# Performance work log

Hardware: AMD Instinct MI355X
Metric: run time of the kernel (lower is better)

## Reference

```python
import jax, jax.numpy as jnp
import numpy as np
from jax import lax

L = 3  # num_layers
H = 256  # hidden_size == embedding_size
V = 32000  # vocab (input_size / output_size)


def _lstm_layer(x, h0, c0, Wih, Whh, bih, bhh):
    # x: [T, B, H_in]; PyTorch gate order: i, f, g, o
    b = bih + bhh
    def step(carry, xt):
        h, c = carry
        gates = xt @ Wih.T + h @ Whh.T + b  # [B, 4H]
        i, f, g, o = jnp.split(gates, 4, axis=-1)
        c = jax.nn.sigmoid(f) * c + jax.nn.sigmoid(i) * jnp.tanh(g)
        h = jax.nn.sigmoid(o) * jnp.tanh(c)
        return (h, c), h
    (h, c), ys = lax.scan(step, (h0, c0), x)
    return ys, h, c


def _run_lstm(x, h0, c0, Wih, Whh, bih, bhh):
    hs, cs = [], []
    for l in range(L):
        x, h, c = _lstm_layer(x, h0[l], c0[l], Wih[l], Whh[l], bih[l], bhh[l])
        hs.append(h)
        cs.append(c)
    return x, jnp.stack(hs), jnp.stack(cs)


def setup_inputs() -> dict:
    key = jax.random.key(0)
    ks = jax.random.split(key, 16)
    s = 0.06  # ~ 1/sqrt(H) uniform scale of PyTorch LSTM init
    T_in, T_out, B = 64, 64, 64
    return {
        "inputs": jax.random.randint(ks[0], (T_in, B), 0, V, dtype=jnp.int64),
        "targets": jax.random.randint(ks[1], (T_out, B), 0, V, dtype=jnp.int64),
        "enc_emb": jax.random.normal(ks[2], (V, H), jnp.float32),
        "enc_Wih": jax.random.normal(ks[3], (L, 4 * H, H), jnp.float32) * s,
        "enc_Whh": jax.random.normal(ks[4], (L, 4 * H, H), jnp.float32) * s,
        "enc_bih": jax.random.normal(ks[5], (L, 4 * H), jnp.float32) * s,
        "enc_bhh": jax.random.normal(ks[6], (L, 4 * H), jnp.float32) * s,
        "hidden0": jax.random.normal(ks[7], (L, 1, H), jnp.float32) * s,
        "cell0": jax.random.normal(ks[8], (L, 1, H), jnp.float32) * s,
        "dec_emb": jax.random.normal(ks[9], (V, H), jnp.float32),
        "dec_Wih": jax.random.normal(ks[10], (L, 4 * H, H), jnp.float32) * s,
        "dec_Whh": jax.random.normal(ks[11], (L, 4 * H, H), jnp.float32) * s,
        "dec_bih": jax.random.normal(ks[12], (L, 4 * H), jnp.float32) * s,
        "dec_bhh": jax.random.normal(ks[13], (L, 4 * H), jnp.float32) * s,
        "fc_W": jax.random.normal(ks[14], (V, H), jnp.float32) * s,
        "fc_b": jax.random.normal(ks[15], (V,), jnp.float32) * s,
    }


def reference(inputs, targets, enc_emb, enc_Wih, enc_Whh, enc_bih, enc_bhh,
              hidden0, cell0, dec_emb, dec_Wih, dec_Whh, dec_bih, dec_bhh,
              fc_W, fc_b):
    B = inputs.shape[-1]
    # Encoder: learned init state broadcast over batch
    h0 = jnp.broadcast_to(hidden0, (L, B, H))
    c0 = jnp.broadcast_to(cell0, (L, B, H))
    x = enc_emb[inputs]  # [T_in, B, H]
    _, h, c = _run_lstm(x, h0, c0, enc_Wih, enc_Whh, enc_bih, enc_bhh)
    # Decoder with teacher forcing (teacher_forcing_prob=1):
    # decoder_in = targets shifted right with zero start token
    dec_in = jnp.concatenate([jnp.zeros((1, B), targets.dtype), targets[:-1]], axis=0)
    y = dec_emb[dec_in]  # [T_out, B, H]
    y, _, _ = _run_lstm(y, h, c, dec_Wih, dec_Whh, dec_bih, dec_bhh)
    decoder_out = y @ fc_W.T + fc_b  # [T_out, B, V]
    predicted_words = jnp.argmax(decoder_out, axis=-1)
    return decoder_out, predicted_words
```

## Files before the change

### kernel.cpp

```cpp
#include <hip/hip_runtime.h>
#include <math.h>

#define TT   64
#define BB   64
#define HH   256
#define VV   32000
#define NG   1024
#define KK   256

typedef __bf16 bf16x8 __attribute__((ext_vector_type(8)));
typedef float  f32x4  __attribute__((ext_vector_type(4)));

__global__ void embed_kernel(const int* __restrict__ tok, const float* __restrict__ tab,
                             float* __restrict__ X, int shifted) {
  int blk = blockIdx.x;
  int t = blk >> 6, b = blk & 63;
  int id;
  if (shifted) id = (t == 0) ? 0 : tok[(t - 1) * BB + b];
  else         id = tok[t * BB + b];
  const float4* src = (const float4*)(tab + (long)id * HH);
  float4* dst = (float4*)(X + (long)blk * HH);
  dst[threadIdx.x] = src[threadIdx.x];
}

__global__ void pack_wih(const float* __restrict__ eW, const float* __restrict__ dW,
                         const float* __restrict__ ebi, const float* __restrict__ ebh,
                         const float* __restrict__ dbi, const float* __restrict__ dbh,
                         float* __restrict__ Wpk, float* __restrict__ bpk) {
  int L = blockIdx.y;
  int rp = blockIdx.x;
  int j = rp >> 2, g = rp & 3;
  int r = g * HH + j;
  const float* src = (L < 3 ? eW + (long)L * NG * HH : dW + (long)(L - 3) * NG * HH) + (long)r * HH;
  float* dst = Wpk + ((long)L * NG + rp) * HH;
  ((float4*)dst)[threadIdx.x] = ((const float4*)src)[threadIdx.x];
  if (threadIdx.x == 0) {
    const float* bi = (L < 3 ? ebi + L * NG : dbi + (L - 3) * NG);
    const float* bh = (L < 3 ? ebh + L * NG : dbh + (L - 3) * NG);
    bpk[(long)L * NG + rp] = bi[r] + bh[r];
  }
}

__global__ void pack_whhT(const float* __restrict__ eW, const float* __restrict__ dW,
                          float* __restrict__ WT) {
  int L = blockIdx.y;
  int k = blockIdx.x;
  const float* src = (L < 3 ? eW + (long)L * NG * HH : dW + (long)(L - 3) * NG * HH);
  float* dst = WT + ((long)L * HH + k) * NG;
  int t = threadIdx.x;
  float4 v;
  v.x = src[((long)(0 * HH + t)) * HH + k];
  v.y = src[((long)(1 * HH + t)) * HH + k];
  v.z = src[((long)(2 * HH + t)) * HH + k];
  v.w = src[((long)(3 * HH + t)) * HH + k];
  ((float4*)dst)[t] = v;
}

__device__ __forceinline__ unsigned long long shfl_xor_u64(unsigned long long v, int m) {
  unsigned lo = (unsigned)v, hi = (unsigned)(v >> 32);
  lo = __shfl_xor(lo, m);
  hi = __shfl_xor(hi, m);
  return ((unsigned long long)hi << 32) | lo;
}

__device__ __forceinline__ unsigned bf_rne(float x) {
  unsigned u = __float_as_uint(x);
  return (u + 0x7FFFu + ((u >> 16) & 1u)) >> 16;
}
__device__ __forceinline__ void bf_split4(float4 v, short4& hi, short4& lo) {
  unsigned h0 = bf_rne(v.x), h1 = bf_rne(v.y), h2 = bf_rne(v.z), h3 = bf_rne(v.w);
  hi = make_short4((short)h0, (short)h1, (short)h2, (short)h3);
  lo = make_short4((short)bf_rne(v.x - __uint_as_float(h0 << 16)),
                   (short)bf_rne(v.y - __uint_as_float(h1 << 16)),
                   (short)bf_rne(v.z - __uint_as_float(h2 << 16)),
                   (short)bf_rne(v.w - __uint_as_float(h3 << 16)));
}

__global__ __launch_bounds__(256) void gemm_mfma(
    const float* __restrict__ A, const float* __restrict__ B,
    const float* __restrict__ bias, float* __restrict__ C,
    int N, unsigned long long* __restrict__ amax) {
  __shared__ short lds[4 * 128 * 64];
  short* Ah = lds;
  short* Al = Ah + 128 * 64;
  short* Bh = Al + 128 * 64;
  short* Bl = Bh + 128 * 64;
  const int t = threadIdx.x;
  const int lane = t & 63;
  const int wid = t >> 6;
  const int wm = wid >> 1, wn = wid & 1;
  const int lx = lane & 15, lg = lane >> 4;
  const int m0 = blockIdx.y * 128, n0 = blockIdx.x * 128;
  f32x4 acc[4][4] = {};

  for (int kc = 0; kc < KK; kc += 64) {
    #pragma unroll
    for (int p = 0; p < 8; p++) {
      int f   = t + 256 * p;
      int row = f >> 4;
      int c4  = f & 15;
      float4 av = *(const float4*)(A + (long)(m0 + row) * KK + kc + c4 * 4);
      float4 bv = *(const float4*)(B + (long)(n0 + row) * KK + kc + c4 * 4);
      int boff = row * 128 + ((c4 * 8) ^ ((row & 7) << 4));
      short4 h4, l4;
      bf_split4(av, h4, l4);
      *(short4*)((char*)Ah + boff) = h4;
      *(short4*)((char*)Al + boff) = l4;
      bf_split4(bv, h4, l4);
      *(short4*)((char*)Bh + boff) = h4;
      *(short4*)((char*)Bl + boff) = l4;
    }
    __syncthreads();
    #pragma unroll
    for (int ks = 0; ks < 2; ks++) {
      bf16x8 ah[4], al[4], bh[4], bl[4];
      #pragma unroll
      for (int q = 0; q < 4; q++) {
        int ra = wm * 64 + q * 16 + lx;
        int ca = (ks * 64 + lg * 16) ^ ((ra & 7) << 4);
        ah[q] = *(const bf16x8*)((const char*)Ah + ra * 128 + ca);
        al[q] = *(const bf16x8*)((const char*)Al + ra * 128 + ca);
        int rb = wn * 64 + q * 16 + lx;
        int cb = (ks * 64 + lg * 16) ^ ((rb & 7) << 4);
        bh[q] = *(const bf16x8*)((const char*)Bh + rb * 128 + cb);
        bl[q] = *(const bf16x8*)((const char*)Bl + rb * 128 + cb);
      }
      #pragma unroll
      for (int mf = 0; mf < 4; mf++)
        #pragma unroll
        for (int nf = 0; nf < 4; nf++) {
          acc[mf][nf] = __builtin_amdgcn_mfma_f32_16x16x32_bf16(ah[mf], bh[nf], acc[mf][nf], 0, 0, 0);
          acc[mf][nf] = __builtin_amdgcn_mfma_f32_16x16x32_bf16(al[mf], bh[nf], acc[mf][nf], 0, 0, 0);
          acc[mf][nf] = __builtin_amdgcn_mfma_f32_16x16x32_bf16(ah[mf], bl[nf], acc[mf][nf], 0, 0, 0);
        }
    }
    __syncthreads();
  }

  float bv[4];
  #pragma unroll
  for (int nf = 0; nf < 4; nf++) bv[nf] = bias[n0 + wn * 64 + nf * 16 + lx];
  #pragma unroll
  for (int mf = 0; mf < 4; mf++) {
    #pragma unroll
    for (int r = 0; r < 4; r++) {
      int m = m0 + wm * 64 + mf * 16 + lg * 4 + r;
      float best = -3.0e38f; int bi = 0;
      #pragma unroll
      for (int nf = 0; nf < 4; nf++) {
        int col = n0 + wn * 64 + nf * 16 + lx;
        float o = acc[mf][nf][r] + bv[nf];
        C[(long)m * N + col] = o;
        if (o > best) { best = o; bi = col; }
      }
      if (amax) {
        unsigned uo = __float_as_uint(best);
        uo = (uo >> 31) ? ~uo : (uo | 0x80000000u);
        unsigned long long key = ((unsigned long long)uo << 32) | (unsigned)(0xFFFFFFFFu - bi);
        #pragma unroll
        for (int s2 = 1; s2 < 16; s2 <<= 1) {
          unsigned long long o2 = shfl_xor_u64(key, s2);
          if (o2 > key) key = o2;
        }
        if (lx == 0) amax[(long)m * 500 + blockIdx.x * 2 + wn] = key;
      }
    }
  }
}

__global__ void argmax_fin(const unsigned long long* __restrict__ amax,
                           float* __restrict__ out1, int ntiles) {
  int row = blockIdx.x;
  int t = threadIdx.x;
  unsigned long long key = 0ull;
  for (int c = t; c < ntiles; c += 64) {
    unsigned long long k = amax[(long)row * ntiles + c];
    if (k > key) key = k;
  }
  #pragma unroll
  for (int s = 1; s < 64; s <<= 1) {
    unsigned long long o = shfl_xor_u64(key, s);
    if (o > key) key = o;
  }
  if (t == 0) out1[row] = (float)(0xFFFFFFFFu - (unsigned)(key & 0xFFFFFFFFu));
}

__global__ __launch_bounds__(1024) void lstm_recur(
    const float* __restrict__ G, const float* __restrict__ WT,
    const float* __restrict__ h0, int h0s,
    const float* __restrict__ c0, int c0s,
    float* __restrict__ Hout, float* __restrict__ hfin, float* __restrict__ cfin) {
  __shared__ float h_lds[HH];
  __shared__ float4 part[3][HH];
  int b = blockIdx.x;
  int j = threadIdx.x & 255;
  int s = threadIdx.x >> 8;
  int k0 = s * 64;
  float c = 0.f;
  if (s == 0) {
    c = c0[b * c0s + j];
    h_lds[j] = h0[b * h0s + j];
  }
  __syncthreads();
  const float4* WT4 = (const float4*)WT;
  for (int t = 0; t < TT; t++) {
    float4 acc;
    if (s == 0) acc = ((const float4*)(G + ((long)(t * BB + b)) * NG))[j];
    else { acc.x = 0.f; acc.y = 0.f; acc.z = 0.f; acc.w = 0.f; }
    #pragma unroll 4
    for (int k = k0; k < k0 + 64; k += 4) {
      float4 h4 = *(const float4*)&h_lds[k];
      float4 w0 = WT4[(long)(k + 0) * HH + j];
      float4 w1 = WT4[(long)(k + 1) * HH + j];
      float4 w2 = WT4[(long)(k + 2) * HH + j];
      float4 w3 = WT4[(long)(k + 3) * HH + j];
      acc.x += h4.x * w0.x; acc.y += h4.x * w0.y; acc.z += h4.x * w0.z; acc.w += h4.x * w0.w;
      acc.x += h4.y * w1.x; acc.y += h4.y * w1.y; acc.z += h4.y * w1.z; acc.w += h4.y * w1.w;
      acc.x += h4.z * w2.x; acc.y += h4.z * w2.y; acc.z += h4.z * w2.z; acc.w += h4.z * w2.w;
      acc.x += h4.w * w3.x; acc.y += h4.w * w3.y; acc.z += h4.w * w3.z; acc.w += h4.w * w3.w;
    }
    if (s) part[s - 1][j] = acc;
    __syncthreads();
    if (s == 0) {
      float4 p1 = part[0][j], p2 = part[1][j], p3 = part[2][j];
      float gi = acc.x + p1.x + p2.x + p3.x;
      float gf = acc.y + p1.y + p2.y + p3.y;
      float gg = acc.z + p1.z + p2.z + p3.z;
      float go = acc.w + p1.w + p2.w + p3.w;
      float i_ = 1.f / (1.f + expf(-gi));
      float f_ = 1.f / (1.f + expf(-gf));
      float g_ = tanhf(gg);
      float o_ = 1.f / (1.f + expf(-go));
      c = f_ * c + i_ * g_;
      float hn = o_ * tanhf(c);
      h_lds[j] = hn;
      Hout[((long)(t * BB + b)) * HH + j] = hn;
    }
    __syncthreads();
  }
  if (s == 0) {
    hfin[b * HH + j] = h_lds[j];
    cfin[b * HH + j] = c;
  }
}

extern "C" void kernel_launch(void* const* d_in, const int* in_sizes, int n_in,
                              void* d_out, int out_size, void* d_ws, size_t ws_size,
                              hipStream_t stream) {
  const int*   inputs  = (const int*)d_in[0];
  const int*   targets = (const int*)d_in[1];
  const float* enc_emb = (const float*)d_in[2];
  const float* enc_Wih = (const float*)d_in[3];
  const float* enc_Whh = (const float*)d_in[4];
  const float* enc_bih = (const float*)d_in[5];
  const float* enc_bhh = (const float*)d_in[6];
  const float* hidden0 = (const float*)d_in[7];
  const float* cell0   = (const float*)d_in[8];
  const float* dec_emb = (const float*)d_in[9];
  const float* dec_Wih = (const float*)d_in[10];
  const float* dec_Whh = (const float*)d_in[11];
  const float* dec_bih = (const float*)d_in[12];
  const float* dec_bhh = (const float*)d_in[13];
  const float* fc_W    = (const float*)d_in[14];
  const float* fc_b    = (const float*)d_in[15];

  float* out0 = (float*)d_out;
  float* out1 = out0 + (long)TT * BB * VV;

  float* X   = (float*)d_ws;
  float* G   = X   + (long)4096 * 256;
  float* Wpk = G   + (long)4096 * 1024;
  float* WT  = Wpk + (long)6 * 1024 * 256;
  float* bpk = WT  + (long)6 * 256 * 1024;
  float* hst = bpk + 6 * 1024;
  float* cst = hst + 3 * 64 * 256;
  float* hsc = cst + 3 * 64 * 256;
  float* csc = hsc + 64 * 256;
  unsigned long long* amax = (unsigned long long*)G;

  embed_kernel<<<4096, 64, 0, stream>>>(inputs, enc_emb, X, 0);
  pack_wih<<<dim3(1024, 6), 64, 0, stream>>>(enc_Wih, dec_Wih, enc_bih, enc_bhh,
                                             dec_bih, dec_bhh, Wpk, bpk);
  pack_whhT<<<dim3(256, 6), 256, 0, stream>>>(enc_Whh, dec_Whh, WT);

  for (int l = 0; l < 3; l++) {
    gemm_mfma<<<dim3(8, 32), 256, 0, stream>>>(X, Wpk + (long)l * NG * HH,
                                               bpk + l * NG, G, NG, nullptr);
    lstm_recur<<<64, 1024, 0, stream>>>(G, WT + (long)l * HH * NG,
                                        hidden0 + l * HH, 0, cell0 + l * HH, 0,
                                        X, hst + (long)l * BB * HH, cst + (long)l * BB * HH);
  }

  embed_kernel<<<4096, 64, 0, stream>>>(targets, dec_emb, X, 1);
  for (int l = 0; l < 3; l++) {
    gemm_mfma<<<dim3(8, 32), 256, 0, stream>>>(X, Wpk + (long)(3 + l) * NG * HH,
                                               bpk + (3 + l) * NG, G, NG, nullptr);
    lstm_recur<<<64, 1024, 0, stream>>>(G, WT + (long)(3 + l) * HH * NG,
                                        hst + (long)l * BB * HH, HH,
                                        cst + (long)l * BB * HH, HH,
                                        X, hsc, csc);
  }

  gemm_mfma<<<dim3(250, 32), 256, 0, stream>>>(X, fc_W, fc_b, out0, VV, amax);
  argmax_fin<<<4096, 64, 0, stream>>>(amax, out1, 500);
}
```

Before: 4.148 ms.

## Spread LSTM recurrence across 128 blocks with register-resident weights and grid barrier

Replaces the per-batch-row recurrence kernel with a cooperative kernel. Each of 128 blocks owns a 16-column slice of the hidden units for 8 batch rows and keeps its recurrent weight slice in registers. Blocks exchange the hidden state through a double-buffered global array and synchronise each timestep with an atomic-counter grid barrier. The old kernel re-read the whole recurrent weight matrix from cache on every step, and this change is meant to remove that traffic. It also switches to fast exp-based sigmoid and tanh. The barrier relies on all 128 blocks being resident at once, and it adds per-step global synchronisation latency.

```diff
diff --git a/kernel.cpp b/kernel.cpp
--- a/kernel.cpp
+++ b/kernel.cpp
@@ -7,6 +7,8 @@
 #define VV   32000
 #define NG   1024
 #define KK   256
+
+#define NBLK_R 128
 
 typedef __bf16 bf16x8 __attribute__((ext_vector_type(8)));
 typedef float  f32x4  __attribute__((ext_vector_type(4)));
@@ -185,62 +187,102 @@
   if (t == 0) out1[row] = (float)(0xFFFFFFFFu - (unsigned)(key & 0xFFFFFFFFu));
 }
 
-__global__ __launch_bounds__(1024) void lstm_recur(
-    const float* __restrict__ G, const float* __restrict__ WT,
+__global__ void init_bar(unsigned* bar) {
+  if (threadIdx.x == 0) { bar[0] = 0u; bar[1] = 0u; }
+}
+
+__global__ __launch_bounds__(256) void lstm_recur_coop(
+    const float* __restrict__ G,
+    const float* __restrict__ WTl,
     const float* __restrict__ h0, int h0s,
     const float* __restrict__ c0, int c0s,
-    float* __restrict__ Hout, float* __restrict__ hfin, float* __restrict__ cfin) {
-  __shared__ float h_lds[HH];
-  __shared__ float4 part[3][HH];
-  int b = blockIdx.x;
-  int j = threadIdx.x & 255;
-  int s = threadIdx.x >> 8;
-  int k0 = s * 64;
-  float c = 0.f;
-  if (s == 0) {
-    c = c0[b * c0s + j];
-    h_lds[j] = h0[b * h0s + j];
-  }
+    float* __restrict__ Hout,
+    float* __restrict__ hfin, float* __restrict__ cfin,
+    float* __restrict__ hT_g,
+    unsigned* __restrict__ bar,
+    unsigned gen0) {
+  __shared__ f32x4 part[8][16][16];
+  const int tid = threadIdx.x;
+  const int s = tid >> 4;
+  const int j = tid & 15;
+  const int js = blockIdx.x & 15, bg = blockIdx.x >> 4;
+  const int jg = js * 16 + j;
+  const int k0 = s * 16;
+
+  f32x4 w[16];
+  #pragma unroll
+  for (int kk = 0; kk < 16; kk++)
+    w[kk] = *(const f32x4*)(WTl + (long)(k0 + kk) * NG + jg * 4);
+
+  for (int idx = tid; idx < 2048; idx += 256) {
+    int k = idx >> 3, b = idx & 7;
+    hT_g[((long)(0 * 8 + bg) * HH + k) * 8 + b] = h0[(long)(bg * 8 + b) * h0s + k];
+  }
+
+  float c_state = 0.f;
+  if (tid < 128) c_state = c0[(long)(bg * 8 + s) * c0s + jg];
   __syncthreads();
-  const float4* WT4 = (const float4*)WT;
+
   for (int t = 0; t < TT; t++) {
-    float4 acc;
-    if (s == 0) acc = ((const float4*)(G + ((long)(t * BB + b)) * NG))[j];
-    else { acc.x = 0.f; acc.y = 0.f; acc.z = 0.f; acc.w = 0.f; }
-    #pragma unroll 4
-    for (int k = k0; k < k0 + 64; k += 4) {
-      float4 h4 = *(const float4*)&h_lds[k];
-      float4 w0 = WT4[(long)(k + 0) * HH + j];
-      float4 w1 = WT4[(long)(k + 1) * HH + j];
-      float4 w2 = WT4[(long)(k + 2) * HH + j];
-      float4 w3 = WT4[(long)(k + 3) * HH + j];
-      acc.x += h4.x * w0.x; acc.y += h4.x * w0.y; acc.z += h4.x * w0.z; acc.w += h4.x * w0.w;
-      acc.x += h4.y * w1.x; acc.y += h4.y * w1.y; acc.z += h4.y * w1.z; acc.w += h4.y * w1.w;
-      acc.x += h4.z * w2.x; acc.y += h4.z * w2.y; acc.z += h4.z * w2.z; acc.w += h4.z * w2.w;
-      acc.x += h4.w * w3.x; acc.y += h4.w * w3.y; acc.z += h4.w * w3.z; acc.w += h4.w * w3.w;
-    }
-    if (s) part[s - 1][j] = acc;
+    const int par = t & 1;
+    const float* hb = hT_g + (long)(par * 8 + bg) * (HH * 8);
+
+    f32x4 g4 = {0.f, 0.f, 0.f, 0.f};
+    if (tid < 128)
+      g4 = *(const f32x4*)(G + ((long)t * BB + bg * 8 + s) * NG + jg * 4);
+
+    f32x4 acc[8] = {};
+    #pragma unroll
+    for (int kk = 0; kk < 16; kk++) {
+      const f32x4 wv = w[kk];
+      const f32x4 h0v = *(const f32x4*)(hb + (k0 + kk) * 8);
+      const f32x4 h1v = *(const f32x4*)(hb + (k0 + kk) * 8 + 4);
+      acc[0] += wv * h0v.x; acc[1] += wv * h0v.y;
+      acc[2] += wv * h0v.z; acc[3] += wv * h0v.w;
+      acc[4] += wv * h1v.x; acc[5] += wv * h1v.y;
+      acc[6] += wv * h1v.z; acc[7] += wv * h1v.w;
+    }
+    #pragma unroll
+    for (int b = 0; b < 8; b++) part[b][s][j] = acc[b];
     __syncthreads();
-    if (s == 0) {
-      float4 p1 = part[0][j], p2 = part[1][j], p3 = part[2][j];
-      float gi = acc.x + p1.x + p2.x + p3.x;
-      float gf = acc.y + p1.y + p2.y + p3.y;
-      float gg = acc.z + p1.z + p2.z + p3.z;
-      float go = acc.w + p1.w + p2.w + p3.w;
-      float i_ = 1.f / (1.f + expf(-gi));
-      float f_ = 1.f / (1.f + expf(-gf));
-      float g_ = tanhf(gg);
-      float o_ = 1.f / (1.f + expf(-go));
-      c = f_ * c + i_ * g_;
-      float hn = o_ * tanhf(c);
-      h_lds[j] = hn;
-      Hout[((long)(t * BB + b)) * HH + j] = hn;
-    }
-    __syncthreads();
-  }
-  if (s == 0) {
-    hfin[b * HH + j] = h_lds[j];
-    cfin[b * HH + j] = c;
+
+    if (tid < 128) {
+      f32x4 gs = g4;
+      #pragma unroll
+      for (int ss = 0; ss < 16; ss++) gs += part[s][ss][j];
+      float i_ = 1.f / (1.f + __expf(-gs.x));
+      float f_ = 1.f / (1.f + __expf(-gs.y));
+      float g_ = 2.f / (1.f + __expf(-2.f * gs.z)) - 1.f;
+      float o_ = 1.f / (1.f + __expf(-gs.w));
+      c_state = f_ * c_state + i_ * g_;
+      float th = 2.f / (1.f + __expf(-2.f * c_state)) - 1.f;
+      float hn = o_ * th;
+      Hout[((long)t * BB + bg * 8 + s) * HH + jg] = hn;
+      hT_g[((long)((par ^ 1) * 8 + bg) * HH + jg) * 8 + s] = hn;
+      if (t == TT - 1) {
+        hfin[(long)(bg * 8 + s) * HH + jg] = hn;
+        cfin[(long)(bg * 8 + s) * HH + jg] = c_state;
+      }
+    }
+
+    if (t != TT - 1) {
+      __syncthreads();
+      if (tid == 0) {
+        const unsigned target = gen0 + (unsigned)t + 1u;
+        __threadfence();
+        unsigned prev = __hip_atomic_fetch_add(&bar[0], 1u, __ATOMIC_ACQ_REL,
+                                               __HIP_MEMORY_SCOPE_AGENT);
+        if (prev == (unsigned)(NBLK_R - 1)) {
+          __hip_atomic_store(&bar[0], 0u, __ATOMIC_RELAXED, __HIP_MEMORY_SCOPE_AGENT);
+          __hip_atomic_store(&bar[1], target, __ATOMIC_RELEASE, __HIP_MEMORY_SCOPE_AGENT);
+        } else {
+          while (__hip_atomic_load(&bar[1], __ATOMIC_ACQUIRE, __HIP_MEMORY_SCOPE_AGENT) < target)
+            __builtin_amdgcn_s_sleep(2);
+        }
+        __threadfence();
+      }
+      __syncthreads();
+    }
   }
 }
 
@@ -278,6 +320,11 @@
   float* csc = hsc + 64 * 256;
   unsigned long long* amax = (unsigned long long*)G;
 
+  char* wend = (char*)d_ws + (ws_size & ~(size_t)255);
+  float* hTg = (float*)(wend - (2 * 8 * 256 * 8) * sizeof(float) - 256);
+  unsigned* bar = (unsigned*)(wend - 128);
+
+  init_bar<<<1, 64, 0, stream>>>(bar);
   embed_kernel<<<4096, 64, 0, stream>>>(inputs, enc_emb, X, 0);
   pack_wih<<<dim3(1024, 6), 64, 0, stream>>>(enc_Wih, dec_Wih, enc_bih, enc_bhh,
                                              dec_bih, dec_bhh, Wpk, bpk);
@@ -286,19 +333,21 @@
   for (int l = 0; l < 3; l++) {
     gemm_mfma<<<dim3(8, 32), 256, 0, stream>>>(X, Wpk + (long)l * NG * HH,
                                                bpk + l * NG, G, NG, nullptr);
-    lstm_recur<<<64, 1024, 0, stream>>>(G, WT + (long)l * HH * NG,
-                                        hidden0 + l * HH, 0, cell0 + l * HH, 0,
-                                        X, hst + (long)l * BB * HH, cst + (long)l * BB * HH);
+    lstm_recur_coop<<<NBLK_R, 256, 0, stream>>>(G, WT + (long)l * HH * NG,
+                                                hidden0 + l * HH, 0, cell0 + l * HH, 0,
+                                                X, hst + (long)l * BB * HH, cst + (long)l * BB * HH,
+                                                hTg, bar, (unsigned)(l * 64));
   }
 
   embed_kernel<<<4096, 64, 0, stream>>>(targets, dec_emb, X, 1);
   for (int l = 0; l < 3; l++) {
     gemm_mfma<<<dim3(8, 32), 256, 0, stream>>>(X, Wpk + (long)(3 + l) * NG * HH,
                                                bpk + (3 + l) * NG, G, NG, nullptr);
-    lstm_recur<<<64, 1024, 0, stream>>>(G, WT + (long)(3 + l) * HH * NG,
-                                        hst + (long)l * BB * HH, HH,
-                                        cst + (long)l * BB * HH, HH,
-                                        X, hsc, csc);
+    lstm_recur_coop<<<NBLK_R, 256, 0, stream>>>(G, WT + (long)(3 + l) * HH * NG,
+                                                hst + (long)l * BB * HH, HH,
+                                                cst + (long)l * BB * HH, HH,
+                                                X, hsc, csc,
+                                                hTg, bar, (unsigned)((3 + l) * 64));
   }
 
   gemm_mfma<<<dim3(250, 32), 256, 0, stream>>>(X, fc_W, fc_b, out0, VV, amax);
```

Result: slower. 6.802 ms (+64.0%).

## Keep recurrent LSTM weights register-resident and split K across eight slices

Applied to the files above, without the earlier changes.

The recurrent kernel now loads each thread's slice of the transposed Whh (32 k-rows by 8 gate columns) into registers once, before the time loop, instead of re-reading the weights from global memory or L2 every timestep. Work is split into 8 K-slices of 128 threads, and the partial sums are reduced through a padded LDS buffer. Gate nonlinearities use fast __expf-based sigmoid/tanh, and the final h and c are written inside the last step. This holds 256 floats of weights per thread under a 1024-thread block, which risks register spilling, and the fast math slightly changes numerics.

```diff
diff --git a/kernel.cpp b/kernel.cpp
--- a/kernel.cpp
+++ b/kernel.cpp
@@ -185,62 +185,74 @@
   if (t == 0) out1[row] = (float)(0xFFFFFFFFu - (unsigned)(key & 0xFFFFFFFFu));
 }
 
-__global__ __launch_bounds__(1024) void lstm_recur(
-    const float* __restrict__ G, const float* __restrict__ WT,
+__global__ __launch_bounds__(1024, 4) void lstm_unit(
+    const float* __restrict__ G,
+    const float* __restrict__ WTl,
     const float* __restrict__ h0, int h0s,
     const float* __restrict__ c0, int c0s,
-    float* __restrict__ Hout, float* __restrict__ hfin, float* __restrict__ cfin) {
-  __shared__ float h_lds[HH];
-  __shared__ float4 part[3][HH];
-  int b = blockIdx.x;
-  int j = threadIdx.x & 255;
-  int s = threadIdx.x >> 8;
-  int k0 = s * 64;
-  float c = 0.f;
-  if (s == 0) {
-    c = c0[b * c0s + j];
-    h_lds[j] = h0[b * h0s + j];
+    float* __restrict__ Hout,
+    float* __restrict__ hfin, float* __restrict__ cfin) {
+  __shared__ float h_sh[HH];
+  __shared__ float part2[128 * 72];
+  const int tid = threadIdx.x;
+  const int b = blockIdx.x;
+  const int ks = tid >> 7;
+  const int rw = tid & 127;
+
+  f32x4 w[32][2];
+  #pragma unroll
+  for (int k = 0; k < 32; k++) {
+    const float* wp = WTl + (long)(ks * 32 + k) * NG + rw * 8;
+    w[k][0] = *(const f32x4*)wp;
+    w[k][1] = *(const f32x4*)(wp + 4);
+  }
+
+  float c_state = 0.f;
+  if (tid < HH) {
+    h_sh[tid] = h0[(long)b * h0s + tid];
+    c_state = c0[(long)b * c0s + tid];
   }
   __syncthreads();
-  const float4* WT4 = (const float4*)WT;
+
   for (int t = 0; t < TT; t++) {
-    float4 acc;
-    if (s == 0) acc = ((const float4*)(G + ((long)(t * BB + b)) * NG))[j];
-    else { acc.x = 0.f; acc.y = 0.f; acc.z = 0.f; acc.w = 0.f; }
-    #pragma unroll 4
-    for (int k = k0; k < k0 + 64; k += 4) {
-      float4 h4 = *(const float4*)&h_lds[k];
-      float4 w0 = WT4[(long)(k + 0) * HH + j];
-      float4 w1 = WT4[(long)(k + 1) * HH + j];
-      float4 w2 = WT4[(long)(k + 2) * HH + j];
-      float4 w3 = WT4[(long)(k + 3) * HH + j];
-      acc.x += h4.x * w0.x; acc.y += h4.x * w0.y; acc.z += h4.x * w0.z; acc.w += h4.x * w0.w;
-      acc.x += h4.y * w1.x; acc.y += h4.y * w1.y; acc.z += h4.y * w1.z; acc.w += h4.y * w1.w;
-      acc.x += h4.z * w2.x; acc.y += h4.z * w2.y; acc.z += h4.z * w2.z; acc.w += h4.z * w2.w;
-      acc.x += h4.w * w3.x; acc.y += h4.w * w3.y; acc.z += h4.w * w3.z; acc.w += h4.w * w3.w;
-    }
-    if (s) part[s - 1][j] = acc;
+    f32x4 g4 = {0.f, 0.f, 0.f, 0.f};
+    if (tid < HH)
+      g4 = *(const f32x4*)(G + ((long)t * BB + b) * NG + tid * 4);
+
+    f32x4 a0 = {0.f, 0.f, 0.f, 0.f}, a1 = {0.f, 0.f, 0.f, 0.f};
+    #pragma unroll
+    for (int k4 = 0; k4 < 8; k4++) {
+      f32x4 h4 = *(const f32x4*)&h_sh[ks * 32 + k4 * 4];
+      a0 += w[k4 * 4 + 0][0] * h4.x; a1 += w[k4 * 4 + 0][1] * h4.x;
+      a0 += w[k4 * 4 + 1][0] * h4.y; a1 += w[k4 * 4 + 1][1] * h4.y;
+      a0 += w[k4 * 4 + 2][0] * h4.z; a1 += w[k4 * 4 + 2][1] * h4.z;
+      a0 += w[k4 * 4 + 3][0] * h4.w; a1 += w[k4 * 4 + 3][1] * h4.w;
+    }
+    *(f32x4*)&part2[rw * 72 + ks * 8]     = a0;
+    *(f32x4*)&part2[rw * 72 + ks * 8 + 4] = a1;
     __syncthreads();
-    if (s == 0) {
-      float4 p1 = part[0][j], p2 = part[1][j], p3 = part[2][j];
-      float gi = acc.x + p1.x + p2.x + p3.x;
-      float gf = acc.y + p1.y + p2.y + p3.y;
-      float gg = acc.z + p1.z + p2.z + p3.z;
-      float go = acc.w + p1.w + p2.w + p3.w;
-      float i_ = 1.f / (1.f + expf(-gi));
-      float f_ = 1.f / (1.f + expf(-gf));
-      float g_ = tanhf(gg);
-      float o_ = 1.f / (1.f + expf(-go));
-      c = f_ * c + i_ * g_;
-      float hn = o_ * tanhf(c);
-      h_lds[j] = hn;
-      Hout[((long)(t * BB + b)) * HH + j] = hn;
+
+    if (tid < HH) {
+      f32x4 gs = g4;
+      const int base = (tid >> 1) * 72 + (tid & 1) * 4;
+      #pragma unroll
+      for (int kr = 0; kr < 8; kr++)
+        gs += *(const f32x4*)&part2[base + kr * 8];
+      float i_ = 1.f / (1.f + __expf(-gs.x));
+      float f_ = 1.f / (1.f + __expf(-gs.y));
+      float g_ = 2.f / (1.f + __expf(-2.f * gs.z)) - 1.f;
+      float o_ = 1.f / (1.f + __expf(-gs.w));
+      c_state = f_ * c_state + i_ * g_;
+      float th = 2.f / (1.f + __expf(-2.f * c_state)) - 1.f;
+      float hn = o_ * th;
+      h_sh[tid] = hn;
+      Hout[((long)t * BB + b) * HH + tid] = hn;
+      if (t == TT - 1) {
+        hfin[(long)b * HH + tid] = hn;
+        cfin[(long)b * HH + tid] = c_state;
+      }
     }
     __syncthreads();
-  }
-  if (s == 0) {
-    hfin[b * HH + j] = h_lds[j];
-    cfin[b * HH + j] = c;
   }
 }
 
@@ -286,19 +298,19 @@
   for (int l = 0; l < 3; l++) {
     gemm_mfma<<<dim3(8, 32), 256, 0, stream>>>(X, Wpk + (long)l * NG * HH,
                                                bpk + l * NG, G, NG, nullptr);
-    lstm_recur<<<64, 1024, 0, stream>>>(G, WT + (long)l * HH * NG,
-                                        hidden0 + l * HH, 0, cell0 + l * HH, 0,
-                                        X, hst + (long)l * BB * HH, cst + (long)l * BB * HH);
+    lstm_unit<<<64, 1024, 0, stream>>>(G, WT + (long)l * HH * NG,
+                                       hidden0 + l * HH, 0, cell0 + l * HH, 0,
+                                       X, hst + (long)l * BB * HH, cst + (long)l * BB * HH);
   }
 
   embed_kernel<<<4096, 64, 0, stream>>>(targets, dec_emb, X, 1);
   for (int l = 0; l < 3; l++) {
     gemm_mfma<<<dim3(8, 32), 256, 0, stream>>>(X, Wpk + (long)(3 + l) * NG * HH,
                                                bpk + (3 + l) * NG, G, NG, nullptr);
-    lstm_recur<<<64, 1024, 0, stream>>>(G, WT + (long)(3 + l) * HH * NG,
-                                        hst + (long)l * BB * HH, HH,
-                                        cst + (long)l * BB * HH, HH,
-                                        X, hsc, csc);
+    lstm_unit<<<64, 1024, 0, stream>>>(G, WT + (long)(3 + l) * HH * NG,
+                                       hst + (long)l * BB * HH, HH,
+                                       cst + (long)l * BB * HH, HH,
+                                       X, hsc, csc);
   }
 
   gemm_mfma<<<dim3(250, 32), 256, 0, stream>>>(X, fc_W, fc_b, out0, VV, amax);
```

Measured after the change: 8.459 ms. 104% more time.
